# Optimization experiments

Measured on AMD Instinct MI355X. Metric: run time of the kernel, lower is better.

Reference implementation:

```python
import jax, jax.numpy as jnp
import numpy as np

B, T, N_ITEMS, DIM, L = 512, 50, 10000, 128, 4
H = DIM // 2


def setup_inputs() -> dict:
    key = jax.random.key(0)
    ks = jax.random.split(key, 16)
    emb = jax.random.normal(ks[0], (N_ITEMS + 1, DIM), jnp.float32) * 0.02
    emb = emb.at[0].set(0.0)  # padding_idx=0
    s = 1.0 / np.sqrt(DIM)
    inp = {
        "users": jax.random.randint(ks[1], (B,), 0, B),
        "user_seq": jax.random.randint(ks[2], (B, T), 0, N_ITEMS + 1),
        "pos_items": jax.random.randint(ks[3], (B,), 0, N_ITEMS),
        "neg_items": jax.random.randint(ks[4], (B, 10), 0, N_ITEMS),
        "pos_labels": jnp.ones((B,), jnp.float32),
        "neg_labels": jnp.zeros((B, 10), jnp.float32),
        "base_model_preds": jax.random.normal(ks[5], (B, N_ITEMS), jnp.float32),
        "emb": emb,
        "lstm_wih": jax.random.uniform(ks[6], (4 * DIM, DIM), jnp.float32, -s, s),
        "lstm_whh": jax.random.uniform(ks[7], (4 * DIM, DIM), jnp.float32, -s, s),
        "lstm_bih": jax.random.uniform(ks[8], (4 * DIM,), jnp.float32, -s, s),
        "lstm_bhh": jax.random.uniform(ks[9], (4 * DIM,), jnp.float32, -s, s),
        "wl_W1": jax.random.normal(ks[10], (L, 2 * DIM, H), jnp.float32) * 0.05,
        "wl_b1": jax.random.normal(ks[11], (L, H), jnp.float32) * 0.01,
        "wl_W2": jax.random.normal(ks[12], (L, H), jnp.float32) * 0.05,
        "wl_b2": jax.random.normal(ks[13], (L,), jnp.float32) * 0.01,
        "alphas": jnp.ones((L,), jnp.float32) / L,
    }
    return inp


def _lstm_last(x, wih, whh, bih, bhh):
    # x: [B, T, D]; torch gate order i, f, g, o. Returns last hidden state [B, D].
    Bx, _, D = x.shape
    bias = bih + bhh

    def step(carry, xt):
        h, c = carry
        gates = xt @ wih.T + h @ whh.T + bias  # [B, 4D]
        i, f, g, o = jnp.split(gates, 4, axis=-1)
        c = jax.nn.sigmoid(f) * c + jax.nn.sigmoid(i) * jnp.tanh(g)
        h = jax.nn.sigmoid(o) * jnp.tanh(c)
        return (h, c), None

    init = (jnp.zeros((Bx, D), x.dtype), jnp.zeros((Bx, D), x.dtype))
    (h, _), _ = jax.lax.scan(step, init, x.transpose(1, 0, 2))
    return h


def reference(users, user_seq, pos_items, neg_items, pos_labels, neg_labels,
              base_model_preds, emb, lstm_wih, lstm_whh, lstm_bih, lstm_bhh,
              wl_W1, wl_b1, wl_W2, wl_b2, alphas):
    seq_emb = emb[user_seq]                      # [B, T, D]
    seq_repr = _lstm_last(seq_emb, lstm_wih, lstm_whh, lstm_bih, lstm_bhh)  # [B, D]
    item_emb = emb[jnp.arange(N_ITEMS)]          # [N, D]

    # Weak learners: Linear(2D->H) split algebraically into seq/item matmuls
    # to avoid materializing the [B, N, 2D] broadcast-concat tensor.
    final_scores = jnp.zeros((seq_repr.shape[0], N_ITEMS), seq_repr.dtype)
    for l in range(L):
        sp = seq_repr @ wl_W1[l, :DIM]           # [B, H]
        ip = item_emb @ wl_W1[l, DIM:]           # [N, H]
        hid = jax.nn.relu(sp[:, None, :] + ip[None, :, :] + wl_b1[l])  # [B, N, H]
        scores = hid @ wl_W2[l] + wl_b2[l]       # [B, N]
        final_scores = final_scores + alphas[l] * scores

    pos_scores = jnp.take_along_axis(final_scores, pos_items[:, None], axis=1)  # [B, 1]
    neg_scores = jnp.take_along_axis(final_scores, neg_items, axis=1)           # [B, n_neg]
    loss = jnp.mean(jnp.exp(-(pos_scores - neg_scores)))
    return final_scores, loss
```

## Files before the change

### kernel.cpp

```cpp
#include <hip/hip_runtime.h>
#include <stdint.h>

typedef uint32_t u32;
typedef uint16_t u16;
typedef uint64_t u64;
typedef __attribute__((ext_vector_type(4))) float f32x4;
typedef __attribute__((ext_vector_type(4))) u32 u32x4;
typedef __attribute__((ext_vector_type(8))) short bf16x8;
typedef __attribute__((ext_vector_type(2))) _Float16 f16x2;

#define NI   10000
#define NPAD 10240
#define L2E  1.4426950408889634f

#define DEV static __device__ __forceinline__

DEV float asf(u32 u){ union{u32 i; float f;} v; v.i=u; return v.f; }
DEV u32   asu(float f){ union{u32 i; float f;} v; v.f=f; return v.i; }
DEV float bf2f(u16 u){ return asf(((u32)u)<<16); }
DEV u16   f2bf(float f){ u32 i = asu(f); return (u16)((i + 0x7fffu + ((i>>16)&1u))>>16); }
DEV u16   f2h(float f){ _Float16 h = (_Float16)f; return __builtin_bit_cast(u16, h); }
DEV f16x2 h2c(u32 x){ return __builtin_bit_cast(f16x2, x); }
DEV f32x4 fzero(){ f32x4 z; z[0]=0.f; z[1]=0.f; z[2]=0.f; z[3]=0.f; return z; }

DEV void gl2lds16(const void* g, void* l){
  __builtin_amdgcn_global_load_lds((const __attribute__((address_space(1))) u32*)g,
                                   (__attribute__((address_space(3))) u32*)l, 16, 0, 0);
}

__global__ void k_prep(const int* __restrict__ seq, const float* __restrict__ emb,
                       const float* __restrict__ wih, const float* __restrict__ bih,
                       const float* __restrict__ bhh, const float* __restrict__ W1,
                       const float* __restrict__ b1, const float* __restrict__ W2,
                       const float* __restrict__ alphas,
                       u16* __restrict__ EMB16, u16* __restrict__ Wih16,
                       u16* __restrict__ W1s16, u16* __restrict__ W1i16,
                       float* __restrict__ bias512, float* __restrict__ b1k,
                       u32* __restrict__ w2p)
{
  const int tid = blockIdx.x*blockDim.x + threadIdx.x;
  const int nth = gridDim.x*blockDim.x;
  for (int e = tid; e < 10001*16; e += nth){
    const float* s = emb + (size_t)e*8;
    float4 x0 = *(const float4*)s, x1 = *(const float4*)(s+4);
    bf16x8 o;
    o[0]=(short)f2bf(x0.x); o[1]=(short)f2bf(x0.y); o[2]=(short)f2bf(x0.z); o[3]=(short)f2bf(x0.w);
    o[4]=(short)f2bf(x1.x); o[5]=(short)f2bf(x1.y); o[6]=(short)f2bf(x1.z); o[7]=(short)f2bf(x1.w);
    *(bf16x8*)&EMB16[(size_t)e*8] = o;
  }
  for (int e = tid; e < 512*16; e += nth){
    int col = (e*8)>>7;
    float sc = ((col>>7)==2) ? 2.0f*L2E : L2E;
    const float* s = wih + (size_t)e*8;
    float4 x0 = *(const float4*)s, x1 = *(const float4*)(s+4);
    bf16x8 o;
    o[0]=(short)f2bf(x0.x*sc); o[1]=(short)f2bf(x0.y*sc); o[2]=(short)f2bf(x0.z*sc); o[3]=(short)f2bf(x0.w*sc);
    o[4]=(short)f2bf(x1.x*sc); o[5]=(short)f2bf(x1.y*sc); o[6]=(short)f2bf(x1.z*sc); o[7]=(short)f2bf(x1.w*sc);
    *(bf16x8*)&Wih16[(size_t)e*8] = o;
  }
  for (int e = tid; e < 256*128; e += nth){ int k = e>>7, d = e&127; int l = k>>6, h = k&63;
      W1s16[e] = f2bf(W1[l*16384 + d*64 + h]); }
  for (int e = tid; e < 256*128; e += nth){ int k = e>>7, d = e&127; int l = k>>6, h = k&63;
      W1i16[e] = f2bf(W1[l*16384 + (128+d)*64 + h]); }
  for (int e = tid; e < 512; e += nth){
      float sc = ((e>>7)==2) ? 2.0f*L2E : L2E;
      bias512[e] = (bih[e] + bhh[e])*sc; }
  for (int e = tid; e < 256; e += nth){ int l = e>>6, h = e&63;
      b1k[e] = b1[l*64 + h]; }
  for (int e = tid; e < 128; e += nth){
      int k0 = 2*e, k1 = 2*e+1;
      float w0 = alphas[k0>>6]*W2[(k0>>6)*64 + (k0&63)];
      float w1 = alphas[k1>>6]*W2[(k1>>6)*64 + (k1&63)];
      w2p[e] = (u32)f2h(w0) | ((u32)f2h(w1)<<16); }
}

template<int OUT_MODE, int BIAS_MODE>
DEV void gemm_body(const u16* __restrict__ A, const u16* __restrict__ BT,
                   const float* __restrict__ bias, void* __restrict__ Cout,
                   int Nvalid, int ldc, int bx, int by, char* smem,
                   const int* __restrict__ seq)
{
  u16* sA = (u16*)smem;
  u16* sB = (u16*)(smem + 32768);
  const int tid = threadIdx.x, l = tid&63, w = tid>>6;
  const int c16 = l&15, g4 = l>>4;
  const int m0 = bx*128, n0 = by*64;
  #pragma unroll
  for (int it=0; it<4; ++it){
    int row = it*32 + w*4 + g4;
    int sg  = c16 ^ (row&7);
    if constexpr (OUT_MODE==4){
      int b = (m0&511) + row, t = m0>>9;
      int idx = seq[b*50 + t];
      gl2lds16(A + (size_t)idx*128 + sg*8, (char*)sA + (it*32 + w*4)*256);
    } else {
      gl2lds16(A + (size_t)(m0+row)*128 + sg*8, (char*)sA + (it*32 + w*4)*256);
    }
  }
  #pragma unroll
  for (int it=0; it<2; ++it){
    int row = it*32 + w*4 + g4;
    int srow;
    if constexpr (OUT_MODE==4){
      int base1 = (by>>2)*256 + (by&3)*32;
      srow = base1 + (row&31) + (row>>5)*128;
    } else {
      srow = n0 + row; if (srow >= Nvalid) srow = Nvalid-1;
    }
    int sg  = c16 ^ (row&7);
    gl2lds16(BT + (size_t)srow*128 + sg*8, (char*)sB + (it*32 + w*4)*256);
  }
  __syncthreads();
  f32x4 acc[4];
  #pragma unroll
  for (int ct=0; ct<4; ++ct) acc[ct] = fzero();
  #pragma unroll
  for (int kt=0; kt<4; ++kt){
    bf16x8 a, b[4];
    int arow = w*16 + c16;
    a = *(const bf16x8*)((const char*)sA + arow*256 + (((kt*4+g4) ^ (arow&7))*16));
    #pragma unroll
    for (int ct=0; ct<4; ++ct){
      int brow = (OUT_MODE==4) ? ((ct>>1)*32 + (ct&1)*16 + c16) : (ct*16 + c16);
      b[ct] = *(const bf16x8*)((const char*)sB + brow*256 + (((kt*4+g4) ^ (brow&7))*16));
    }
    #pragma unroll
    for (int ct=0; ct<4; ++ct)
      acc[ct] = __builtin_amdgcn_mfma_f32_16x16x32_bf16(a, b[ct], acc[ct], 0, 0, 0);
  }
  const int rbase = m0 + w*16 + g4*4;
  if constexpr (OUT_MODE==4){
    int t    = rbase >> 9;
    int bloc = rbase & 511;
    int bb   = bloc >> 4;
    int g4l  = (bloc >> 2) & 3;
    int half = by >> 2;
    #pragma unroll
    for (int p=0; p<2; ++p){
      int colA = (by&3)*32 + p*16 + c16 + (by>>2)*256;
      int colB = colA + 128;
      u32 ws[4];
      #pragma unroll
      for (int i=0;i<4;++i){
        float va = acc[p][i], vb = acc[p+2][i];
        if constexpr (BIAS_MODE==1){ va += bias[colA]; vb += bias[colB]; }
        ws[i] = (u32)f2bf(va) | ((u32)f2bf(vb)<<16);
      }
      int tidl = ((by&3)*2 + p)*64 + g4l*16 + c16;
      char* dst = (char*)Cout + ((size_t)((t*32+bb)*1024 + half*512 + tidl))*16;
      *(f32x4*)dst = *(f32x4*)ws;
    }
  } else {
    #pragma unroll
    for (int ct=0; ct<4; ++ct){
      int col = n0 + ct*16 + c16;
      if (col < Nvalid){
        float v[4];
        #pragma unroll
        for (int i=0;i<4;++i){
          v[i] = acc[ct][i];
          if constexpr (BIAS_MODE==1) v[i] += bias[col];
          else if constexpr (BIAS_MODE==2) v[i] += bias[rbase+i];
        }
        if constexpr (OUT_MODE==0){
          float* C = (float*)Cout;
          #pragma unroll
          for (int i=0;i<4;++i) C[(size_t)(rbase+i)*ldc + col] = v[i];
        } else if constexpr (OUT_MODE==1){
          u16* C = (u16*)Cout;
          #pragma unroll
          for (int i=0;i<4;++i) C[(size_t)(rbase+i)*ldc + col] = f2h(v[i]);
        } else {
          u32* C = (u32*)Cout;
          u32 w0 = (u32)f2h(v[0]) | ((u32)f2h(v[1])<<16);
          u32 w1 = (u32)f2h(v[2]) | ((u32)f2h(v[3])<<16);
          int kp0 = rbase>>1;
          C[(size_t)kp0*ldc + col]     = w0;
          C[(size_t)(kp0+1)*ldc + col] = w1;
        }
      }
    }
  }
}

template<int OUT_MODE, int BIAS_MODE>
__global__ __launch_bounds__(512) void k_gemm(const u16* __restrict__ A,
    const u16* __restrict__ BT, const float* __restrict__ bias,
    void* __restrict__ Cout, int Nvalid, int ldc, const int* __restrict__ seq)
{
  __shared__ __align__(16) char smem[49152];
  gemm_body<OUT_MODE,BIAS_MODE>(A, BT, bias, Cout, Nvalid, ldc, blockIdx.x, blockIdx.y, smem, seq);
}

DEV void lstm_body(const float* __restrict__ whh, const u16* __restrict__ XWL,
                   u16* __restrict__ H16, int bb, char* smem)
{
  const int tid = threadIdx.x, l = tid&63, w = tid>>6;
  const int c16 = l&15, g4 = l>>4;
  const int u = w*16 + c16;
  bf16x8 bfr[4][4];
  #pragma unroll
  for (int j=0; j<4; ++j){
    int col = (j*8 + w)*16 + c16;
    float sc = (j==2) ? 2.0f*L2E : L2E;
    const float* src = whh + (size_t)col*128;
    #pragma unroll
    for (int kt=0; kt<4; ++kt){
      int k0 = kt*32 + g4*8;
      float4 x0 = *(const float4*)(src + k0);
      float4 x1 = *(const float4*)(src + k0 + 4);
      bf16x8 f;
      f[0]=(short)f2bf(x0.x*sc); f[1]=(short)f2bf(x0.y*sc); f[2]=(short)f2bf(x0.z*sc); f[3]=(short)f2bf(x0.w*sc);
      f[4]=(short)f2bf(x1.x*sc); f[5]=(short)f2bf(x1.y*sc); f[6]=(short)f2bf(x1.z*sc); f[7]=(short)f2bf(x1.w*sc);
      bfr[kt][j] = f;
    }
  }
  for (int e = tid; e < 4096; e += 512) ((u16*)smem)[e] = 0;
  int hoff[4];
  #pragma unroll
  for (int i=0;i<4;++i){ int s = g4*4 + i;
    hoff[i] = s*256 + (((u>>3) ^ (s&7))*16) + (u&7)*2; }
  const char* gb = (const char*)XWL;
  {
    size_t base = (size_t)bb*1024;
    gl2lds16(gb + (base + tid)*16,        smem + 8192 + w*1024);
    gl2lds16(gb + (base + 512 + tid)*16,  smem + 8192 + 8192 + w*1024);
  }
  float cst[4] = {0.f,0.f,0.f,0.f};
  float hreg[4] = {0.f,0.f,0.f,0.f};
  __syncthreads();
  #pragma unroll 2
  for (int t=0; t<50; ++t){
    const int cur = t&1;
    char* AhC = smem + cur*4096;
    char* AhN = smem + (cur^1)*4096;
    char* XsC = smem + 8192 + cur*16384;
    char* XsN = smem + 8192 + (cur^1)*16384;
    if (t < 49){
      size_t base = (size_t)((t+1)*32+bb)*1024;
      gl2lds16(gb + (base + tid)*16,       XsN + w*1024);
      gl2lds16(gb + (base + 512 + tid)*16, XsN + 8192 + w*1024);
    }
    bf16x8 xv0 = *(const bf16x8*)(XsC + tid*16);
    bf16x8 xv1 = *(const bf16x8*)(XsC + 8192 + tid*16);
    const u32* W0 = (const u32*)&xv0;
    const u32* W1 = (const u32*)&xv1;
    f32x4 acc[4];
    #pragma unroll
    for (int i=0;i<4;++i){
      acc[0][i] = asf(W0[i]<<16);
      acc[1][i] = asf(W0[i]&0xffff0000u);
      acc[2][i] = asf(W1[i]<<16);
      acc[3][i] = asf(W1[i]&0xffff0000u);
    }
    #pragma unroll
    for (int kt=0; kt<4; ++kt){
      bf16x8 a = *(const bf16x8*)(AhC + c16*256 + (((kt*4+g4) ^ (c16&7))*16));
      #pragma unroll
      for (int j=0; j<4; ++j)
        acc[j] = __builtin_amdgcn_mfma_f32_16x16x32_bf16(a, bfr[kt][j], acc[j], 0, 0, 0);
    }
    #pragma unroll
    for (int i=0;i<4;++i){
      float yi = acc[0][i], yf = acc[1][i], yg = acc[2][i], yo = acc[3][i];
      yg = fminf(fmaxf(yg, -40.f), 40.f);
      float Ei = __builtin_amdgcn_exp2f(-yi);
      float Ef = __builtin_amdgcn_exp2f(-yf);
      float G  = __builtin_amdgcn_exp2f(yg);
      float Eo = __builtin_amdgcn_exp2f(-yo);
      float ai = 1.f+Ei, af = 1.f+Ef, gp = G+1.f, gm = G-1.f;
      float num = fmaf(af, gm, cst[i]*ai*gp);
      float den = af*ai*gp;
      float cn  = num * __builtin_amdgcn_rcpf(den);
      cst[i] = cn;
      float yc = fminf(fmaxf(cn*(2.0f*L2E), -40.f), 40.f);
      float C2 = __builtin_amdgcn_exp2f(yc);
      float h  = (C2-1.f) * __builtin_amdgcn_rcpf((1.f+Eo)*(C2+1.f));
      hreg[i] = h;
      *(u16*)(AhN + hoff[i]) = f2bf(h);
    }
    __syncthreads();
  }
  #pragma unroll
  for (int i=0;i<4;++i)
    H16[(size_t)(bb*16 + g4*4 + i)*128 + u] = f2bf(hreg[i]);
}

__global__ __launch_bounds__(512) void k_lstm_ipf(const float* __restrict__ whh,
    const u16* __restrict__ XWL, u16* __restrict__ H16,
    const u16* __restrict__ W1i16, const u16* __restrict__ EMB16,
    const float* __restrict__ b1k, u32* __restrict__ IPF)
{
  __shared__ __align__(16) char smem[49152];
  if (blockIdx.x < 32){
    lstm_body(whh, XWL, H16, blockIdx.x, smem);
  } else {
    int g = blockIdx.x - 32;
    gemm_body<2,2>(W1i16, EMB16, b1k, IPF, NI, NPAD, g&1, g>>1, smem, nullptr);
  }
}

__global__ __launch_bounds__(512) void k_post(const u16* __restrict__ H16,
    const u16* __restrict__ W1s16, u16* __restrict__ SPH)
{
  __shared__ __align__(16) char smem[49152];
  gemm_body<1,0>(H16, W1s16, nullptr, SPH, 256, 256, blockIdx.x&3, blockIdx.x>>2, smem, nullptr);
}

DEV float fdot2(u32 ab, u32 w, float acc){
  asm("v_dot2_f32_f16 %0, %1, %2, %0" : "+v"(acc) : "v"(ab), "s"(w));
  return acc;
}
DEV u32 pkmax0(u32 t){
  u32 r; asm("v_pk_max_f16 %0, %1, 0" : "=v"(r) : "v"(t)); return r;
}

__global__ __launch_bounds__(256) void k_score(const u32* __restrict__ SPH,
    const u32* __restrict__ IPF, const u32* __restrict__ w2p,
    const float* __restrict__ alphas, const float* __restrict__ b2,
    float* __restrict__ out)
{
  __shared__ __align__(16) u32 sp_lds[8*128];
  const int tid = threadIdx.x;
  const int n  = blockIdx.x*256 + tid;
  const int b0 = blockIdx.y*8;
  {
    const u32* src = SPH + (size_t)b0*128 + tid*4;
    *(u32x4*)&sp_lds[tid*4] = *(const u32x4*)src;
  }
  float cb2 = 0.f;
  #pragma unroll
  for (int ll=0;ll<4;++ll) cb2 += alphas[ll]*b2[ll];
  __syncthreads();
  float acc[8];
  #pragma unroll
  for (int i=0;i<8;++i) acc[i] = cb2;
  #pragma unroll 1
  for (int c=0;c<4;++c){
    u32 iw[32];
    #pragma unroll
    for (int v=0; v<32; ++v) iw[v] = IPF[(size_t)(c*32+v)*NPAD + n];
    const u32* wp = w2p + c*32;
    #pragma unroll
    for (int i=0;i<8;++i){
      float a = acc[i];
      #pragma unroll
      for (int vq=0; vq<8; ++vq){
        u32x4 sp4 = *(const u32x4*)&sp_lds[i*128 + c*32 + vq*4];
        #pragma unroll
        for (int q=0;q<4;++q){
          f16x2 t = h2c(sp4[q]) + h2c(iw[vq*4+q]);
          u32 r = pkmax0(__builtin_bit_cast(u32, t));
          a = fdot2(r, wp[vq*4+q], a);
        }
      }
      acc[i] = a;
    }
  }
  if (n < NI){
    #pragma unroll
    for (int i=0;i<8;++i) out[(size_t)(b0+i)*NI + n] = acc[i];
  }
}

__global__ void k_loss(const float* __restrict__ scores, const int* __restrict__ pos,
                       const int* __restrict__ neg, float* __restrict__ outloss)
{
  __shared__ float red[256];
  int tid = threadIdx.x;
  float s = 0.f;
  for (int e = tid; e < 5120; e += 256){
    int b = e/10, j = e - b*10;
    float ps = scores[(size_t)b*NI + pos[b]];
    float ns = scores[(size_t)b*NI + neg[b*10 + j]];
    s += __expf(ns - ps);
  }
  red[tid] = s; __syncthreads();
  for (int st=128; st>0; st>>=1){ if (tid<st) red[tid]+=red[tid+st]; __syncthreads(); }
  if (tid==0) outloss[0] = red[0] * (1.0f/5120.0f);
}

extern "C" void kernel_launch(void* const* d_in, const int* in_sizes, int n_in,
                              void* d_out, int out_size, void* d_ws, size_t ws_size,
                              hipStream_t stream)
{
  const int*   seq    = (const int*)d_in[1];
  const int*   pos    = (const int*)d_in[2];
  const int*   neg    = (const int*)d_in[3];
  const float* emb    = (const float*)d_in[7];
  const float* wih    = (const float*)d_in[8];
  const float* whh    = (const float*)d_in[9];
  const float* bih    = (const float*)d_in[10];
  const float* bhh    = (const float*)d_in[11];
  const float* W1     = (const float*)d_in[12];
  const float* b1     = (const float*)d_in[13];
  const float* W2     = (const float*)d_in[14];
  const float* b2     = (const float*)d_in[15];
  const float* alphas = (const float*)d_in[16];
  float* out = (float*)d_out;
  (void)in_sizes; (void)n_in; (void)out_size; (void)ws_size;

  char* p = (char*)d_ws;
  size_t off = 0;
  auto alloc = [&](size_t bytes)->char*{ char* r = p + off;
      off = (off + bytes + 255) & ~(size_t)255; return r; };
  u16*  EMB16   = (u16*)  alloc((size_t)10001*128*2);
  u16*  Wih16   = (u16*)  alloc((size_t)512*128*2);
  u16*  W1s16   = (u16*)  alloc((size_t)256*128*2);
  u16*  W1i16   = (u16*)  alloc((size_t)256*128*2);
  float* bias512= (float*)alloc(512*4);
  float* b1k    = (float*)alloc(256*4);
  u32*  w2p     = (u32*)  alloc(128*4);
  u16*  XWL     = (u16*)  alloc((size_t)25600*512*2);
  u16*  H16     = (u16*)  alloc((size_t)512*128*2);
  u16*  SPH     = (u16*)  alloc((size_t)512*256*2);
  u32*  IPF     = (u32*)  alloc((size_t)128*NPAD*4);

  k_prep<<<512,256,0,stream>>>(seq, emb, wih, bih, bhh, W1, b1, W2, alphas,
                               EMB16, Wih16, W1s16, W1i16, bias512, b1k, w2p);
  k_gemm<4,1><<<dim3(200,8),512,0,stream>>>(EMB16, Wih16, bias512, XWL, 512, 512, seq);
  k_lstm_ipf<<<32 + 314,512,0,stream>>>(whh, XWL, H16, W1i16, EMB16, b1k, IPF);
  k_post<<<16,512,0,stream>>>(H16, W1s16, SPH);
  k_score<<<dim3(40,64),256,0,stream>>>((const u32*)SPH, IPF, w2p, alphas, b2, out);
  k_loss<<<1,256,0,stream>>>(out, pos, neg, out + (size_t)512*NI);
}
```

Baseline: 163.3 us.

## Move k_score's weighted hidden-unit reduction onto MFMA with a zero-padded B operand

In k_score, the per-pair v_dot2 accumulation over hidden units is replaced by one 16x16x32 f16 MFMA per chunk. The relu'd (sp+ip) values become the A operand and the w2 weights fill only column 0 of B. The work split also changes: each wave now handles 16 items across 64 users, keeps the IPF slices in registers and reads SPH straight from global memory instead of LDS, with a new grid shape. The aim is to cut VALU instruction count per score, at the cost of using only 1/16 of the MFMA output and writing results from 4 lanes per wave as 16-byte stores.

Result: slower. 183.9 us (+12.6%).

```diff
diff --git a/kernel.cpp b/kernel.cpp
--- a/kernel.cpp
+++ b/kernel.cpp
@@ -7,6 +7,7 @@
 typedef __attribute__((ext_vector_type(4))) float f32x4;
 typedef __attribute__((ext_vector_type(4))) u32 u32x4;
 typedef __attribute__((ext_vector_type(8))) short bf16x8;
+typedef __attribute__((ext_vector_type(8))) _Float16 f16x8;
 typedef __attribute__((ext_vector_type(2))) _Float16 f16x2;
 
 #define NI   10000
@@ -307,10 +308,6 @@
   gemm_body<1,0>(H16, W1s16, nullptr, SPH, 256, 256, blockIdx.x&3, blockIdx.x>>2, smem, nullptr);
 }
 
-DEV float fdot2(u32 ab, u32 w, float acc){
-  asm("v_dot2_f32_f16 %0, %1, %2, %0" : "+v"(acc) : "v"(ab), "s"(w));
-  return acc;
-}
 DEV u32 pkmax0(u32 t){
   u32 r; asm("v_pk_max_f16 %0, %1, 0" : "=v"(r) : "v"(t)); return r;
 }
@@ -320,46 +317,53 @@
     const float* __restrict__ alphas, const float* __restrict__ b2,
     float* __restrict__ out)
 {
-  __shared__ __align__(16) u32 sp_lds[8*128];
-  const int tid = threadIdx.x;
-  const int n  = blockIdx.x*256 + tid;
-  const int b0 = blockIdx.y*8;
-  {
-    const u32* src = SPH + (size_t)b0*128 + tid*4;
-    *(u32x4*)&sp_lds[tid*4] = *(const u32x4*)src;
+  const int tid = threadIdx.x, l = tid&63, w = tid>>6;
+  const int g4 = l>>4, r16 = l&15;
+  const int n0 = blockIdx.x*16;
+  const int b0 = (blockIdx.y*4 + w)*64;
+  u32x4 bfr[8];
+  #pragma unroll
+  for (int c=0;c<8;++c){
+    u32x4 v;
+    #pragma unroll
+    for (int jj=0;jj<4;++jj)
+      v[jj] = (r16==0) ? w2p[c*16 + g4*4 + jj] : 0u;
+    bfr[c] = v;
+  }
+  u32x4 ipf[8];
+  #pragma unroll
+  for (int c=0;c<8;++c){
+    u32x4 v;
+    #pragma unroll
+    for (int jj=0;jj<4;++jj)
+      v[jj] = IPF[(size_t)(c*16 + g4*4 + jj)*NPAD + (n0 + r16)];
+    ipf[c] = v;
   }
   float cb2 = 0.f;
   #pragma unroll
   for (int ll=0;ll<4;++ll) cb2 += alphas[ll]*b2[ll];
-  __syncthreads();
-  float acc[8];
-  #pragma unroll
-  for (int i=0;i<8;++i) acc[i] = cb2;
-  #pragma unroll 1
-  for (int c=0;c<4;++c){
-    u32 iw[32];
-    #pragma unroll
-    for (int v=0; v<32; ++v) iw[v] = IPF[(size_t)(c*32+v)*NPAD + n];
-    const u32* wp = w2p + c*32;
-    #pragma unroll
-    for (int i=0;i<8;++i){
-      float a = acc[i];
+  #pragma unroll 2
+  for (int b = b0; b < b0+64; ++b){
+    const u32* spb = SPH + (size_t)b*128 + g4*4;
+    u32x4 sp[8];
+    #pragma unroll
+    for (int c=0;c<8;++c) sp[c] = *(const u32x4*)(spb + c*16);
+    f32x4 acc; acc[0]=cb2; acc[1]=cb2; acc[2]=cb2; acc[3]=cb2;
+    #pragma unroll
+    for (int c=0;c<8;++c){
+      u32x4 pa;
       #pragma unroll
-      for (int vq=0; vq<8; ++vq){
-        u32x4 sp4 = *(const u32x4*)&sp_lds[i*128 + c*32 + vq*4];
-        #pragma unroll
-        for (int q=0;q<4;++q){
-          f16x2 t = h2c(sp4[q]) + h2c(iw[vq*4+q]);
-          u32 r = pkmax0(__builtin_bit_cast(u32, t));
-          a = fdot2(r, wp[vq*4+q], a);
-        }
+      for (int jj=0;jj<4;++jj){
+        f16x2 t = h2c(sp[c][jj]) + h2c(ipf[c][jj]);
+        pa[jj] = pkmax0(__builtin_bit_cast(u32, t));
       }
-      acc[i] = a;
-    }
-  }
-  if (n < NI){
-    #pragma unroll
-    for (int i=0;i<8;++i) out[(size_t)(b0+i)*NI + n] = acc[i];
+      acc = __builtin_amdgcn_mfma_f32_16x16x32_f16(
+              __builtin_bit_cast(f16x8, pa),
+              __builtin_bit_cast(f16x8, bfr[c]),
+              acc, 0, 0, 0);
+    }
+    if (r16 == 0)
+      *(f32x4*)&out[(size_t)b*NI + n0 + g4*4] = acc;
   }
 }
 
@@ -421,6 +425,6 @@
   k_gemm<4,1><<<dim3(200,8),512,0,stream>>>(EMB16, Wih16, bias512, XWL, 512, 512, seq);
   k_lstm_ipf<<<32 + 314,512,0,stream>>>(whh, XWL, H16, W1i16, EMB16, b1k, IPF);
   k_post<<<16,512,0,stream>>>(H16, W1s16, SPH);
-  k_score<<<dim3(40,64),256,0,stream>>>((const u32*)SPH, IPF, w2p, alphas, b2, out);
+  k_score<<<dim3(625,2),256,0,stream>>>((const u32*)SPH, IPF, w2p, alphas, b2, out);
   k_loss<<<1,256,0,stream>>>(out, pos, neg, out + (size_t)512*NI);
 }
```
